# Performance work log

Hardware: AMD Instinct MI355X
Metric: run time of the kernel (lower is better)

The kernel has to match this reference:

```python
import jax, jax.numpy as jnp
import numpy as np

N = 100000   # nodes
E = 800000   # edges (avg degree 8)
D = 64       # in_feats == n_hidden
L = 3        # n_layers
BN_EPS = 1e-5


def _l2norm(h):
    # F.normalize(dim=-1), eps=1e-12
    n = jnp.linalg.norm(h, axis=-1, keepdims=True)
    return h / jnp.maximum(n, 1e-12)


def setup_inputs() -> dict:
    key = jax.random.key(0)
    ks = jax.random.split(key, 16)
    s = 0.05
    x = jax.random.uniform(ks[0], (N, D), dtype=jnp.float32) * 10.0  # count-like, nonneg
    edge_src = jax.random.randint(ks[1], (E,), 0, N, dtype=jnp.int32)
    edge_dst = jax.random.randint(ks[2], (E,), 0, N, dtype=jnp.int32)
    return {
        "x": x,
        "edge_src": edge_src,
        "edge_dst": edge_dst,
        "W_self": jax.random.normal(ks[3], (L, D, D), jnp.float32) * s,
        "W_neigh": jax.random.normal(ks[4], (L, D, D), jnp.float32) * s,
        "b_sage": jnp.zeros((L, D), jnp.float32),
        "fc_w": jax.random.normal(ks[5], (D, D), jnp.float32) * s,
        "fc_b": jnp.zeros((D,), jnp.float32),
        "bn_gamma": jnp.ones((D,), jnp.float32),
        "bn_beta": jnp.zeros((D,), jnp.float32),
        "bn_mean": jax.random.normal(ks[6], (D,), jnp.float32) * 0.1,
        "bn_var": jax.random.uniform(ks[7], (D,), jnp.float32) + 0.5,
        "fc21_w": jax.random.normal(ks[8], (D, D), jnp.float32) * s,
        "fc21_b": jnp.zeros((D,), jnp.float32),
        "fc22_w": jax.random.normal(ks[9], (D, D), jnp.float32) * s,
        "fc22_b": jnp.zeros((D,), jnp.float32),
    }


def reference(x, edge_src, edge_dst, W_self, W_neigh, b_sage, fc_w, fc_b,
              bn_gamma, bn_beta, bn_mean, bn_var, fc21_w, fc21_b, fc22_w, fc22_b):
    n = x.shape[0]
    h = jnp.log(x + 1.0)
    # mean-aggregator degree normalization (clamped at 1 like DGL)
    deg = jax.ops.segment_sum(jnp.ones(edge_dst.shape, h.dtype), edge_dst, num_segments=n)
    deg = jnp.maximum(deg, 1.0)[:, None]
    for l in range(L):
        neigh = jax.ops.segment_sum(h[edge_src], edge_dst, num_segments=n) / deg
        h = h @ W_self[l] + neigh @ W_neigh[l] + b_sage[l]
        if l < L - 1:  # last SAGEConv has no activation / norm
            h = _l2norm(jax.nn.relu(h))
    # fc head: Linear -> BatchNorm1d(eval) -> ReLU -> Softplus
    h = h @ fc_w + fc_b
    h = (h - bn_mean) * jax.lax.rsqrt(bn_var + BN_EPS) * bn_gamma + bn_beta
    h = jax.nn.relu(h)
    h = jax.nn.softplus(h)
    z_loc = h @ fc21_w + fc21_b
    z_scale = jnp.exp(h @ fc22_w + fc22_b)
    return (z_loc, z_scale)
```

## Files before the change

### kernel.cpp

```cpp
#include <hip/hip_runtime.h>
#include <math.h>

#define NN 100000
#define NE 800000
#define NB 512
#define EPB 4096

typedef short bf16x8 __attribute__((ext_vector_type(8)));
typedef float f32x4 __attribute__((ext_vector_type(4)));
typedef unsigned short u16x8 __attribute__((ext_vector_type(8)));
typedef unsigned short u16x4 __attribute__((ext_vector_type(4)));

__device__ __forceinline__ float bf2f(unsigned short u) {
    union { unsigned u32; float f; } c; c.u32 = ((unsigned)u) << 16; return c.f;
}
__device__ __forceinline__ unsigned short f2bf(float f) {
    union { float f; unsigned u; } c; c.f = f;
    unsigned u = c.u;
    unsigned r = (u + 0x7fffu + ((u >> 16) & 1u)) >> 16;
    return (unsigned short)r;
}
__device__ __forceinline__ int bucket_of(int d) {
    return (int)(((long long)d * NB) / NN);
}
__device__ __forceinline__ int node_start_of(int b) {
    return (int)(((long long)b * NN) / NB);
}


__global__ void zero_kernel(int* __restrict__ gcount) {
    int i = blockIdx.x * 256 + threadIdx.x;
    if (i < NB) gcount[i] = 0;
}

__global__ __launch_bounds__(256) void bucket_hist_kernel(
        const int* __restrict__ dst, int* __restrict__ gcount) {
    __shared__ int hist[NB];
    int e0 = blockIdx.x * EPB;
    int e1 = min(e0 + EPB, NE);
    for (int i = threadIdx.x; i < NB; i += 256) hist[i] = 0;
    __syncthreads();
    for (int e = e0 + threadIdx.x; e < e1; e += 256)
        atomicAdd(&hist[bucket_of(dst[e])], 1);
    __syncthreads();
    for (int i = threadIdx.x; i < NB; i += 256)
        if (hist[i]) atomicAdd(&gcount[i], hist[i]);
}

__global__ __launch_bounds__(512) void bucket_scan_kernel(
        const int* __restrict__ gcount, int* __restrict__ bucket_base,
        int* __restrict__ gcursor) {
    __shared__ int ws[8];
    int t = threadIdx.x, lane = t & 63, w = t >> 6;
    int v = gcount[t];
    int incl = v;
    #pragma unroll
    for (int off = 1; off < 64; off <<= 1) { int s = __shfl_up(incl, off); if (lane >= off) incl += s; }
    if (lane == 63) ws[w] = incl;
    __syncthreads();
    int woff = 0;
    for (int i = 0; i < w; i++) woff += ws[i];
    int excl = woff + incl - v;
    bucket_base[t] = excl;
    gcursor[t] = 0;
    if (t == NB - 1) bucket_base[NB] = excl + v;
}

__global__ __launch_bounds__(256) void bin_edges_kernel(
        const int* __restrict__ src, const int* __restrict__ dst,
        const int* __restrict__ bucket_base, int* __restrict__ gcursor,
        int* __restrict__ pairs) {
    __shared__ int hist[NB];
    __shared__ int base[NB];
    int e0 = blockIdx.x * EPB;
    int e1 = min(e0 + EPB, NE);
    for (int i = threadIdx.x; i < NB; i += 256) hist[i] = 0;
    __syncthreads();
    for (int e = e0 + threadIdx.x; e < e1; e += 256)
        atomicAdd(&hist[bucket_of(dst[e])], 1);
    __syncthreads();
    for (int i = threadIdx.x; i < NB; i += 256) {
        int c = hist[i];
        base[i] = c ? atomicAdd(&gcursor[i], c) : 0;
        hist[i] = 0;
    }
    __syncthreads();
    for (int e = e0 + threadIdx.x; e < e1; e += 256) {
        int d = dst[e];
        int b = bucket_of(d);
        int li = d - node_start_of(b);
        int r = atomicAdd(&hist[b], 1);
        unsigned idx = (unsigned)(bucket_base[b] + base[b] + r);
        if (idx < NE) pairs[idx] = (src[e] << 8) | li;
    }
}

__global__ __launch_bounds__(256) void csr_place_kernel(
        const int* __restrict__ pairs, const int* __restrict__ bucket_base,
        int* __restrict__ row_ptr, int* __restrict__ col) {
    int b = blockIdx.x;
    int ns = node_start_of(b);
    int cnt = node_start_of(b + 1) - ns;
    __shared__ int cur[200];
    __shared__ int off[200];
    int eb = bucket_base[b], ee = bucket_base[b + 1];
    for (int i = threadIdx.x; i < cnt; i += 256) cur[i] = 0;
    __syncthreads();
    for (int p = eb + threadIdx.x; p < ee; p += 256) {
        int li = pairs[p] & 255;
        if (li < cnt) atomicAdd(&cur[li], 1);
    }
    __syncthreads();
    if (threadIdx.x == 0) {
        int run = 0;
        for (int i = 0; i < cnt; i++) { off[i] = run; run += cur[i]; }
    }
    __syncthreads();
    for (int i = threadIdx.x; i < cnt; i += 256) {
        row_ptr[ns + i] = eb + off[i];
        cur[i] = 0;
    }
    if (b == NB - 1 && threadIdx.x == 0) row_ptr[NN] = NE;
    __syncthreads();
    for (int p = eb + threadIdx.x; p < ee; p += 256) {
        int pr = pairs[p];
        int li = pr & 255;
        if (li < cnt) {
            int pos = atomicAdd(&cur[li], 1);
            unsigned q = (unsigned)(eb + off[li] + pos);
            if (q < NE) col[q] = pr >> 8;
        }
    }
}


__global__ void pack_w_kernel(const float* __restrict__ Wself, const float* __restrict__ Wneigh,
                              const float* __restrict__ fcw, const float* __restrict__ w21,
                              const float* __restrict__ w22, unsigned short* __restrict__ pack) {
    int tid = blockIdx.x * 256 + threadIdx.x;
    if (tid >= 9 * 4096) return;
    int m = tid / 4096, r = tid % 4096;
    int e = r & 7, l = (r >> 3) & 63, kb = (r >> 9) & 1, nt = r >> 10;
    int k = kb * 32 + (l >> 4) * 8 + e;
    int n = nt * 16 + (l & 15);
    const float* src;
    if (m < 3) src = Wself + m * 4096;
    else if (m < 6) src = Wneigh + (m - 3) * 4096;
    else if (m == 6) src = fcw;
    else if (m == 7) src = w21;
    else src = w22;
    pack[tid] = f2bf(src[k * 64 + n]);
}


__global__ void log1p_kernel(const float* __restrict__ x, unsigned short* __restrict__ h) {
    int i = blockIdx.x * 256 + threadIdx.x;
    if (i < NN * 16) {
        float4 v = ((const float4*)x)[i];
        u16x4 o;
        o[0] = f2bf(__logf(v.x + 1.f)); o[1] = f2bf(__logf(v.y + 1.f));
        o[2] = f2bf(__logf(v.z + 1.f)); o[3] = f2bf(__logf(v.w + 1.f));
        ((u16x4*)h)[i] = o;
    }
}


template <bool ACT>
__global__ __launch_bounds__(256) void agg_sage_kernel(
        const unsigned short* __restrict__ hc, unsigned short* __restrict__ hn,
        const int* __restrict__ row_ptr, const int* __restrict__ col,
        const unsigned short* __restrict__ packS, const unsigned short* __restrict__ packN,
        const float* __restrict__ bias) {
    __shared__ unsigned short tl[4][16][72];
    int wid = threadIdx.x >> 6, l = threadIdx.x & 63;
    int row_base = blockIdx.x * 64 + wid * 16;
    int slot = l >> 3;
    int f = (l & 7) * 8;

    for (int i = 0; i < 16; i++) {
        int node = row_base + i;
        if (node >= NN) break;
        int beg = row_ptr[node], end = row_ptr[node + 1];
        float a0 = 0.f, a1 = 0.f, a2 = 0.f, a3 = 0.f, a4 = 0.f, a5 = 0.f, a6 = 0.f, a7 = 0.f;
        for (int p = beg + slot; p < end; p += 16) {
            int p1 = p + 8;
            unsigned s0 = min((unsigned)col[p], (unsigned)(NN - 1));
            u16x8 v0 = *(const u16x8*)(hc + (size_t)s0 * 64 + f);
            if (p1 < end) {
                unsigned s1 = min((unsigned)col[p1], (unsigned)(NN - 1));
                u16x8 v1 = *(const u16x8*)(hc + (size_t)s1 * 64 + f);
                a0 += bf2f(v1[0]); a1 += bf2f(v1[1]); a2 += bf2f(v1[2]); a3 += bf2f(v1[3]);
                a4 += bf2f(v1[4]); a5 += bf2f(v1[5]); a6 += bf2f(v1[6]); a7 += bf2f(v1[7]);
            }
            a0 += bf2f(v0[0]); a1 += bf2f(v0[1]); a2 += bf2f(v0[2]); a3 += bf2f(v0[3]);
            a4 += bf2f(v0[4]); a5 += bf2f(v0[5]); a6 += bf2f(v0[6]); a7 += bf2f(v0[7]);
        }
        #pragma unroll
        for (int off = 8; off < 64; off <<= 1) {
            a0 += __shfl_xor(a0, off); a1 += __shfl_xor(a1, off);
            a2 += __shfl_xor(a2, off); a3 += __shfl_xor(a3, off);
            a4 += __shfl_xor(a4, off); a5 += __shfl_xor(a5, off);
            a6 += __shfl_xor(a6, off); a7 += __shfl_xor(a7, off);
        }
        if (l < 8) {
            float inv = 1.f / fmaxf((float)(end - beg), 1.f);
            u16x8 o;
            o[0] = f2bf(a0 * inv); o[1] = f2bf(a1 * inv); o[2] = f2bf(a2 * inv); o[3] = f2bf(a3 * inv);
            o[4] = f2bf(a4 * inv); o[5] = f2bf(a5 * inv); o[6] = f2bf(a6 * inv); o[7] = f2bf(a7 * inv);
            *(u16x8*)(&tl[wid][i][f]) = o;
        }
    }

    int arow = row_base + (l & 15);
    int koff = (l >> 4) * 8;
    bf16x8 z = {0, 0, 0, 0, 0, 0, 0, 0};
    bf16x8 aS0 = z, aS1 = z;
    if (arow < NN) {
        const unsigned short* hp = hc + (size_t)arow * 64 + koff;
        aS0 = *(const bf16x8*)(hp);
        aS1 = *(const bf16x8*)(hp + 32);
    }
    bf16x8 aN0 = *(const bf16x8*)(&tl[wid][l & 15][koff]);
    bf16x8 aN1 = *(const bf16x8*)(&tl[wid][l & 15][32 + koff]);
    int col0 = l & 15;
    int ro4 = (l >> 4) * 4;
    float ss0 = 0.f, ss1 = 0.f, ss2 = 0.f, ss3 = 0.f;
    f32x4 accs[4];
    #pragma unroll
    for (int nt = 0; nt < 4; nt++) {
        bf16x8 b0 = *(const bf16x8*)(packS + ((nt * 2 + 0) * 64 + l) * 8);
        bf16x8 b1 = *(const bf16x8*)(packS + ((nt * 2 + 1) * 64 + l) * 8);
        bf16x8 c0 = *(const bf16x8*)(packN + ((nt * 2 + 0) * 64 + l) * 8);
        bf16x8 c1 = *(const bf16x8*)(packN + ((nt * 2 + 1) * 64 + l) * 8);
        f32x4 acc = {0.f, 0.f, 0.f, 0.f};
        acc = __builtin_amdgcn_mfma_f32_16x16x32_bf16(aS0, b0, acc, 0, 0, 0);
        acc = __builtin_amdgcn_mfma_f32_16x16x32_bf16(aS1, b1, acc, 0, 0, 0);
        acc = __builtin_amdgcn_mfma_f32_16x16x32_bf16(aN0, c0, acc, 0, 0, 0);
        acc = __builtin_amdgcn_mfma_f32_16x16x32_bf16(aN1, c1, acc, 0, 0, 0);
        float bv = bias[nt * 16 + col0];
        #pragma unroll
        for (int j = 0; j < 4; j++) {
            float v = acc[j] + bv;
            if (ACT) {
                v = fmaxf(v, 0.f);
                if (j == 0) ss0 = fmaf(v, v, ss0);
                if (j == 1) ss1 = fmaf(v, v, ss1);
                if (j == 2) ss2 = fmaf(v, v, ss2);
                if (j == 3) ss3 = fmaf(v, v, ss3);
            }
            acc[j] = v;
        }
        accs[nt] = acc;
    }
    if (ACT) {
        #pragma unroll
        for (int off = 1; off < 16; off <<= 1) {
            ss0 += __shfl_xor(ss0, off); ss1 += __shfl_xor(ss1, off);
            ss2 += __shfl_xor(ss2, off); ss3 += __shfl_xor(ss3, off);
        }
        float i0 = 1.f / fmaxf(sqrtf(ss0), 1e-12f);
        float i1 = 1.f / fmaxf(sqrtf(ss1), 1e-12f);
        float i2 = 1.f / fmaxf(sqrtf(ss2), 1e-12f);
        float i3 = 1.f / fmaxf(sqrtf(ss3), 1e-12f);
        #pragma unroll
        for (int nt = 0; nt < 4; nt++) {
            accs[nt][0] *= i0; accs[nt][1] *= i1; accs[nt][2] *= i2; accs[nt][3] *= i3;
        }
    }
    #pragma unroll
    for (int j = 0; j < 4; j++) {
        int row = row_base + ro4 + j;
        if (row < NN) {
            #pragma unroll
            for (int nt = 0; nt < 4; nt++)
                hn[(size_t)row * 64 + nt * 16 + col0] = f2bf(accs[nt][j]);
        }
    }
}

__global__ __launch_bounds__(256) void head_mfma_kernel(
        const unsigned short* __restrict__ h,
        const unsigned short* __restrict__ packFC, const float* __restrict__ fc_b,
        const float* __restrict__ bn_g, const float* __restrict__ bn_b,
        const float* __restrict__ bn_m, const float* __restrict__ bn_v,
        const unsigned short* __restrict__ pack21, const float* __restrict__ b21,
        const unsigned short* __restrict__ pack22, const float* __restrict__ b22,
        float* __restrict__ zloc, float* __restrict__ zscale) {
    __shared__ unsigned short tl[4][16][72];
    int wid = threadIdx.x >> 6, l = threadIdx.x & 63;
    int row_base = blockIdx.x * 64 + wid * 16;
    int arow = row_base + (l & 15);
    int koff = (l >> 4) * 8;
    bf16x8 z = {0, 0, 0, 0, 0, 0, 0, 0};
    bf16x8 a0 = z, a1 = z;
    if (arow < NN) {
        const unsigned short* hp = h + (size_t)arow * 64 + koff;
        a0 = *(const bf16x8*)(hp);
        a1 = *(const bf16x8*)(hp + 32);
    }
    int col0 = l & 15;
    int ro4 = (l >> 4) * 4;

    #pragma unroll
    for (int nt = 0; nt < 4; nt++) {
        bf16x8 b0 = *(const bf16x8*)(packFC + ((nt * 2 + 0) * 64 + l) * 8);
        bf16x8 b1 = *(const bf16x8*)(packFC + ((nt * 2 + 1) * 64 + l) * 8);
        f32x4 acc = {0.f, 0.f, 0.f, 0.f};
        acc = __builtin_amdgcn_mfma_f32_16x16x32_bf16(a0, b0, acc, 0, 0, 0);
        acc = __builtin_amdgcn_mfma_f32_16x16x32_bf16(a1, b1, acc, 0, 0, 0);
        int col = nt * 16 + col0;
        float scale = bn_g[col] * rsqrtf(bn_v[col] + 1e-5f);
        float mm = bn_m[col], bb = bn_b[col], fb = fc_b[col];
        #pragma unroll
        for (int j = 0; j < 4; j++) {
            float u = (acc[j] + fb - mm) * scale + bb;
            u = fmaxf(u, 0.f);
            float t = u + __logf(1.f + __expf(-u));
            tl[wid][ro4 + j][col] = f2bf(t);
        }
    }
    __syncthreads();
    bf16x8 t0 = *(const bf16x8*)(&tl[wid][l & 15][koff]);
    bf16x8 t1 = *(const bf16x8*)(&tl[wid][l & 15][32 + koff]);

    #pragma unroll
    for (int nt = 0; nt < 4; nt++) {
        bf16x8 b0 = *(const bf16x8*)(pack21 + ((nt * 2 + 0) * 64 + l) * 8);
        bf16x8 b1 = *(const bf16x8*)(pack21 + ((nt * 2 + 1) * 64 + l) * 8);
        f32x4 acc = {0.f, 0.f, 0.f, 0.f};
        acc = __builtin_amdgcn_mfma_f32_16x16x32_bf16(t0, b0, acc, 0, 0, 0);
        acc = __builtin_amdgcn_mfma_f32_16x16x32_bf16(t1, b1, acc, 0, 0, 0);
        int col = nt * 16 + col0;
        float bv = b21[col];
        #pragma unroll
        for (int j = 0; j < 4; j++) {
            int row = row_base + ro4 + j;
            if (row < NN) zloc[(size_t)row * 64 + col] = acc[j] + bv;
        }
    }

    #pragma unroll
    for (int nt = 0; nt < 4; nt++) {
        bf16x8 b0 = *(const bf16x8*)(pack22 + ((nt * 2 + 0) * 64 + l) * 8);
        bf16x8 b1 = *(const bf16x8*)(pack22 + ((nt * 2 + 1) * 64 + l) * 8);
        f32x4 acc = {0.f, 0.f, 0.f, 0.f};
        acc = __builtin_amdgcn_mfma_f32_16x16x32_bf16(t0, b0, acc, 0, 0, 0);
        acc = __builtin_amdgcn_mfma_f32_16x16x32_bf16(t1, b1, acc, 0, 0, 0);
        int col = nt * 16 + col0;
        float bv = b22[col];
        #pragma unroll
        for (int j = 0; j < 4; j++) {
            int row = row_base + ro4 + j;
            if (row < NN) zscale[(size_t)row * 64 + col] = __expf(acc[j] + bv);
        }
    }
}


extern "C" void kernel_launch(void* const* d_in, const int* in_sizes, int n_in,
                              void* d_out, int out_size, void* d_ws, size_t ws_size,
                              hipStream_t stream) {
    const float* x       = (const float*)d_in[0];
    const int*   esrc    = (const int*)d_in[1];
    const int*   edst    = (const int*)d_in[2];
    const float* W_self  = (const float*)d_in[3];
    const float* W_neigh = (const float*)d_in[4];
    const float* b_sage  = (const float*)d_in[5];
    const float* fc_w    = (const float*)d_in[6];
    const float* fc_b    = (const float*)d_in[7];
    const float* bn_g    = (const float*)d_in[8];
    const float* bn_b    = (const float*)d_in[9];
    const float* bn_m    = (const float*)d_in[10];
    const float* bn_v    = (const float*)d_in[11];
    const float* w21     = (const float*)d_in[12];
    const float* b21     = (const float*)d_in[13];
    const float* w22     = (const float*)d_in[14];
    const float* b22     = (const float*)d_in[15];

    float* zloc   = (float*)d_out;
    float* zscale = zloc + (size_t)NN * 64;

    unsigned short* hb0  = (unsigned short*)d_ws;
    unsigned short* hb1  = hb0 + (size_t)NN * 64;
    unsigned short* pack = hb1 + (size_t)NN * 64;
    int* pairs       = (int*)(pack + 9 * 4096);
    int* row_ptr     = pairs + NE;
    int* col         = row_ptr + NN + 1;
    int* gcount      = col + NE;
    int* bucket_base = gcount + NB;
    int* gcursor     = bucket_base + NB + 1;

    zero_kernel<<<2, 256, 0, stream>>>(gcount);
    bucket_hist_kernel<<<(NE + EPB - 1) / EPB, 256, 0, stream>>>(edst, gcount);
    bucket_scan_kernel<<<1, 512, 0, stream>>>(gcount, bucket_base, gcursor);
    bin_edges_kernel<<<(NE + EPB - 1) / EPB, 256, 0, stream>>>(
        esrc, edst, bucket_base, gcursor, pairs);
    csr_place_kernel<<<NB, 256, 0, stream>>>(pairs, bucket_base, row_ptr, col);

    pack_w_kernel<<<(9 * 4096 + 255) / 256, 256, 0, stream>>>(
        W_self, W_neigh, fc_w, w21, w22, pack);
    log1p_kernel<<<(NN * 16 + 255) / 256, 256, 0, stream>>>(x, hb0);

    const int gemm_grid = (NN + 63) / 64;

    unsigned short* hc = hb0;
    unsigned short* hn = hb1;
    for (int l = 0; l < 3; l++) {
        unsigned short* pS = pack + l * 4096;
        unsigned short* pN = pack + (3 + l) * 4096;
        if (l < 2)
            agg_sage_kernel<true><<<gemm_grid, 256, 0, stream>>>(
                hc, hn, row_ptr, col, pS, pN, b_sage + l * 64);
        else
            agg_sage_kernel<false><<<gemm_grid, 256, 0, stream>>>(
                hc, hn, row_ptr, col, pS, pN, b_sage + l * 64);
        unsigned short* t = hc; hc = hn; hn = t;
    }

    head_mfma_kernel<<<gemm_grid, 256, 0, stream>>>(
        hc, pack + 6 * 4096, fc_b, bn_g, bn_b, bn_m, bn_v,
        pack + 7 * 4096, b21, pack + 8 * 4096, b22, zloc, zscale);
}
```

Baseline: 230.8 us.

## Split neighbor aggregation into a separate per-node kernel before the SAGE MFMA

Moves the mean neighbor aggregation out of the fused SAGE kernel into its own kernel where each wavefront handles one node. The goal is more concurrent gathers than the old fused loop, which walked 16 nodes per wave one after another. In exchange, the aggregated features make a round trip through global memory and each layer gets an extra kernel launch. The MFMA kernel then reads the aggregated rows from the output buffer in place before overwriting them.

```diff
diff --git a/kernel.cpp b/kernel.cpp
--- a/kernel.cpp
+++ b/kernel.cpp
@@ -164,64 +164,66 @@
     }
 }
 
+__global__ __launch_bounds__(256) void aggregate_kernel(
+        const unsigned short* __restrict__ h, const int* __restrict__ row_ptr,
+        const int* __restrict__ col, unsigned short* __restrict__ out) {
+    int gt = blockIdx.x * 256 + threadIdx.x;
+    int node = gt >> 6;
+    if (node >= NN) return;
+    int lane = threadIdx.x & 63;
+    int slot = lane >> 3;
+    int f = (lane & 7) * 8;
+    int beg = row_ptr[node], end = row_ptr[node + 1];
+    float a0 = 0.f, a1 = 0.f, a2 = 0.f, a3 = 0.f, a4 = 0.f, a5 = 0.f, a6 = 0.f, a7 = 0.f;
+    for (int p = beg + slot; p < end; p += 16) {
+        int p1 = p + 8;
+        unsigned s0 = min((unsigned)col[p], (unsigned)(NN - 1));
+        u16x8 v0 = *(const u16x8*)(h + (size_t)s0 * 64 + f);
+        if (p1 < end) {
+            unsigned s1 = min((unsigned)col[p1], (unsigned)(NN - 1));
+            u16x8 v1 = *(const u16x8*)(h + (size_t)s1 * 64 + f);
+            a0 += bf2f(v1[0]); a1 += bf2f(v1[1]); a2 += bf2f(v1[2]); a3 += bf2f(v1[3]);
+            a4 += bf2f(v1[4]); a5 += bf2f(v1[5]); a6 += bf2f(v1[6]); a7 += bf2f(v1[7]);
+        }
+        a0 += bf2f(v0[0]); a1 += bf2f(v0[1]); a2 += bf2f(v0[2]); a3 += bf2f(v0[3]);
+        a4 += bf2f(v0[4]); a5 += bf2f(v0[5]); a6 += bf2f(v0[6]); a7 += bf2f(v0[7]);
+    }
+    #pragma unroll
+    for (int off = 8; off < 64; off <<= 1) {
+        a0 += __shfl_xor(a0, off); a1 += __shfl_xor(a1, off);
+        a2 += __shfl_xor(a2, off); a3 += __shfl_xor(a3, off);
+        a4 += __shfl_xor(a4, off); a5 += __shfl_xor(a5, off);
+        a6 += __shfl_xor(a6, off); a7 += __shfl_xor(a7, off);
+    }
+    if (lane < 8) {
+        float inv = 1.f / fmaxf((float)(end - beg), 1.f);
+        u16x8 o;
+        o[0] = f2bf(a0 * inv); o[1] = f2bf(a1 * inv); o[2] = f2bf(a2 * inv); o[3] = f2bf(a3 * inv);
+        o[4] = f2bf(a4 * inv); o[5] = f2bf(a5 * inv); o[6] = f2bf(a6 * inv); o[7] = f2bf(a7 * inv);
+        *(u16x8*)(out + (size_t)node * 64 + f) = o;
+    }
+}
+
 
 template <bool ACT>
-__global__ __launch_bounds__(256) void agg_sage_kernel(
-        const unsigned short* __restrict__ hc, unsigned short* __restrict__ hn,
-        const int* __restrict__ row_ptr, const int* __restrict__ col,
+__global__ __launch_bounds__(256) void sage_mfma_kernel(
+        const unsigned short* __restrict__ hin, unsigned short* __restrict__ hnb,
         const unsigned short* __restrict__ packS, const unsigned short* __restrict__ packN,
         const float* __restrict__ bias) {
-    __shared__ unsigned short tl[4][16][72];
     int wid = threadIdx.x >> 6, l = threadIdx.x & 63;
     int row_base = blockIdx.x * 64 + wid * 16;
-    int slot = l >> 3;
-    int f = (l & 7) * 8;
-
-    for (int i = 0; i < 16; i++) {
-        int node = row_base + i;
-        if (node >= NN) break;
-        int beg = row_ptr[node], end = row_ptr[node + 1];
-        float a0 = 0.f, a1 = 0.f, a2 = 0.f, a3 = 0.f, a4 = 0.f, a5 = 0.f, a6 = 0.f, a7 = 0.f;
-        for (int p = beg + slot; p < end; p += 16) {
-            int p1 = p + 8;
-            unsigned s0 = min((unsigned)col[p], (unsigned)(NN - 1));
-            u16x8 v0 = *(const u16x8*)(hc + (size_t)s0 * 64 + f);
-            if (p1 < end) {
-                unsigned s1 = min((unsigned)col[p1], (unsigned)(NN - 1));
-                u16x8 v1 = *(const u16x8*)(hc + (size_t)s1 * 64 + f);
-                a0 += bf2f(v1[0]); a1 += bf2f(v1[1]); a2 += bf2f(v1[2]); a3 += bf2f(v1[3]);
-                a4 += bf2f(v1[4]); a5 += bf2f(v1[5]); a6 += bf2f(v1[6]); a7 += bf2f(v1[7]);
-            }
-            a0 += bf2f(v0[0]); a1 += bf2f(v0[1]); a2 += bf2f(v0[2]); a3 += bf2f(v0[3]);
-            a4 += bf2f(v0[4]); a5 += bf2f(v0[5]); a6 += bf2f(v0[6]); a7 += bf2f(v0[7]);
-        }
-        #pragma unroll
-        for (int off = 8; off < 64; off <<= 1) {
-            a0 += __shfl_xor(a0, off); a1 += __shfl_xor(a1, off);
-            a2 += __shfl_xor(a2, off); a3 += __shfl_xor(a3, off);
-            a4 += __shfl_xor(a4, off); a5 += __shfl_xor(a5, off);
-            a6 += __shfl_xor(a6, off); a7 += __shfl_xor(a7, off);
-        }
-        if (l < 8) {
-            float inv = 1.f / fmaxf((float)(end - beg), 1.f);
-            u16x8 o;
-            o[0] = f2bf(a0 * inv); o[1] = f2bf(a1 * inv); o[2] = f2bf(a2 * inv); o[3] = f2bf(a3 * inv);
-            o[4] = f2bf(a4 * inv); o[5] = f2bf(a5 * inv); o[6] = f2bf(a6 * inv); o[7] = f2bf(a7 * inv);
-            *(u16x8*)(&tl[wid][i][f]) = o;
-        }
-    }
-
     int arow = row_base + (l & 15);
     int koff = (l >> 4) * 8;
     bf16x8 z = {0, 0, 0, 0, 0, 0, 0, 0};
-    bf16x8 aS0 = z, aS1 = z;
+    bf16x8 aS0 = z, aS1 = z, aN0 = z, aN1 = z;
     if (arow < NN) {
-        const unsigned short* hp = hc + (size_t)arow * 64 + koff;
+        const unsigned short* hp = hin + (size_t)arow * 64 + koff;
+        const unsigned short* np = hnb + (size_t)arow * 64 + koff;
         aS0 = *(const bf16x8*)(hp);
         aS1 = *(const bf16x8*)(hp + 32);
-    }
-    bf16x8 aN0 = *(const bf16x8*)(&tl[wid][l & 15][koff]);
-    bf16x8 aN1 = *(const bf16x8*)(&tl[wid][l & 15][32 + koff]);
+        aN0 = *(const bf16x8*)(np);
+        aN1 = *(const bf16x8*)(np + 32);
+    }
     int col0 = l & 15;
     int ro4 = (l >> 4) * 4;
     float ss0 = 0.f, ss1 = 0.f, ss2 = 0.f, ss3 = 0.f;
@@ -273,7 +275,7 @@
         if (row < NN) {
             #pragma unroll
             for (int nt = 0; nt < 4; nt++)
-                hn[(size_t)row * 64 + nt * 16 + col0] = f2bf(accs[nt][j]);
+                hnb[(size_t)row * 64 + nt * 16 + col0] = f2bf(accs[nt][j]);
         }
     }
 }
@@ -406,14 +408,15 @@
     unsigned short* hc = hb0;
     unsigned short* hn = hb1;
     for (int l = 0; l < 3; l++) {
+        aggregate_kernel<<<(NN * 64 + 255) / 256, 256, 0, stream>>>(hc, row_ptr, col, hn);
         unsigned short* pS = pack + l * 4096;
         unsigned short* pN = pack + (3 + l) * 4096;
         if (l < 2)
-            agg_sage_kernel<true><<<gemm_grid, 256, 0, stream>>>(
-                hc, hn, row_ptr, col, pS, pN, b_sage + l * 64);
+            sage_mfma_kernel<true><<<gemm_grid, 256, 0, stream>>>(
+                hc, hn, pS, pN, b_sage + l * 64);
         else
-            agg_sage_kernel<false><<<gemm_grid, 256, 0, stream>>>(
-                hc, hn, row_ptr, col, pS, pN, b_sage + l * 64);
+            sage_mfma_kernel<false><<<gemm_grid, 256, 0, stream>>>(
+                hc, hn, pS, pN, b_sage + l * 64);
         unsigned short* t = hc; hc = hn; hn = t;
     }
 
```

Measured after the change: 208.3 us. 1.11x faster.
